# Optimization experiments

Hardware: AMD Instinct MI355X
Metric: run time of the kernel (lower is better)

Reference implementation:

```python
import jax, jax.numpy as jnp
import numpy as np

B, D, H = 4096, 128, 512


def _diffeq(t, y, W1, b1, v1, W2, b2):
    # y: [..., D] -> dy: [..., D]; time enters additively in the hidden layer
    h = jnp.tanh(y @ W1 + t * v1 + b1)
    return h @ W2 + b2


def setup_inputs() -> dict:
    key = jax.random.key(0)
    k = jax.random.split(key, 6)
    return {
        "t": jax.random.uniform(k[0], (), dtype=jnp.float32),
        "y": jax.random.normal(k[1], (B, D), dtype=jnp.float32),
        "logp": jnp.zeros((B, 1), dtype=jnp.float32),
        "W1": jax.random.normal(k[2], (D, H), dtype=jnp.float32) / np.sqrt(D),
        "b1": jnp.zeros((H,), dtype=jnp.float32),
        "v1": jax.random.normal(k[3], (H,), dtype=jnp.float32) / np.sqrt(H),
        "W2": jax.random.normal(k[4], (H, D), dtype=jnp.float32) / np.sqrt(H),
        "b2": jnp.zeros((D,), dtype=jnp.float32),
    }


def reference(t, y, logp, W1, b1, v1, W2, b2):
    # dy = diffeq(t, y)
    dy = _diffeq(t, y, W1, b1, v1, W2, b2)

    # Exact brute-force divergence: trace of per-sample Jacobian d(dy)/dy.
    # Original loops D autograd.grad passes; here a single vmapped jacfwd
    # (D forward-mode tangents) computes the same quantity.
    def f_single(yi):  # yi: [D]
        return _diffeq(t, yi, W1, b1, v1, W2, b2)

    jac = jax.vmap(jax.jacfwd(f_single))(y)          # [B, D, D]
    divergence = jnp.trace(jac, axis1=1, axis2=2)    # [B]
    divergence = divergence[:, None]                 # [B, 1]

    return (dy, -divergence)
```

## Files before the change

kernel.cpp:

```cpp
#include <hip/hip_runtime.h>

#define B_ 4096
#define D_ 128
#define H_ 512

typedef short v8s __attribute__((ext_vector_type(8)));
typedef float v4f __attribute__((ext_vector_type(4)));

__device__ __forceinline__ unsigned short f2bf(float f) {
    unsigned int u = __float_as_uint(f);
    u += 0x7fffu + ((u >> 16) & 1u);
    return (unsigned short)(u >> 16);
}

__global__ __launch_bounds__(256) void prep_kernel(
    const float* __restrict__ y, const float* __restrict__ W1,
    const float* __restrict__ W2,
    unsigned short* __restrict__ yb, unsigned short* __restrict__ W1T,
    unsigned short* __restrict__ W2T, float* __restrict__ s)
{
    __shared__ __align__(16) float smem[8448];
    const int tid = threadIdx.x;
    const int blk = blockIdx.x;

    if (blk < 64) {
        int idx = blk * 256 + tid;
#pragma unroll
        for (int i = 0; i < 8; ++i) {
            int e = idx + i * 16384;
            float4 v = ((const float4*)y)[e];
            ushort4 o;
            o.x = f2bf(v.x); o.y = f2bf(v.y); o.z = f2bf(v.z); o.w = f2bf(v.w);
            ((ushort4*)yb)[e] = o;
        }
    } else if (blk < 192) {
        float (*tile)[33] = (float(*)[33])smem;
        const float* src; unsigned short* dst;
        int srcC, dstC, r0, c0;
        if (blk < 128) {
            int tt = blk - 64;
            src = W1; dst = W1T; srcC = 512; dstC = 128;
            r0 = (tt >> 4) * 32; c0 = (tt & 15) * 32;
        } else {
            int tt = blk - 128;
            src = W2; dst = W2T; srcC = 128; dstC = 512;
            r0 = (tt >> 2) * 32; c0 = (tt & 3) * 32;
        }
        int c = tid & 31, r = tid >> 5;
#pragma unroll
        for (int i = 0; i < 4; ++i)
            tile[r + i * 8][c] = src[(r0 + r + i * 8) * srcC + c0 + c];
        __syncthreads();
        int rw = tid & 31, cw = tid >> 5;
#pragma unroll
        for (int i = 0; i < 4; ++i)
            dst[(c0 + cw + i * 8) * dstC + r0 + rw] = f2bf(tile[rw][cw + i * 8]);
    } else {
        int kbase = (blk - 192) * 64;
        for (int e = tid; e < 8192; e += 256) {
            int kk = e >> 7, i = e & 127;
            smem[kk * 132 + i] = W2[(kbase + kk) * 128 + i];
        }
        __syncthreads();
        int kk = tid >> 2, sub = tid & 3;
        int k = kbase + kk;
        float a = 0.f;
#pragma unroll 8
        for (int j = 0; j < 32; ++j) {
            int i = sub * 32 + j;
            a = fmaf(W1[i * H_ + k], smem[kk * 132 + i], a);
        }
        a += __shfl_xor(a, 1, 64);
        a += __shfl_xor(a, 2, 64);
        if (sub == 0) s[k] = a;
    }
}

__global__ __launch_bounds__(256) void ode_mfma(
    const float* __restrict__ t_, const unsigned short* __restrict__ yb,
    const unsigned short* __restrict__ W1T, const unsigned short* __restrict__ W2T,
    const float* __restrict__ sg, const float* __restrict__ b1g,
    const float* __restrict__ v1g, const float* __restrict__ b2g,
    float* __restrict__ out)
{
    __shared__ __align__(16) unsigned short hsm[16 * 520];
    __shared__ float divp[4][16];

    const int tid  = threadIdx.x;
    const int lane = tid & 63;
    const int wv   = tid >> 6;
    const int m    = lane & 15;
    const int quad = lane >> 4;
    const int row0 = blockIdx.x * 16;
    const float t  = t_[0];

    v8s af[4];
    const v8s* yrow = (const v8s*)&yb[(row0 + m) * D_ + quad * 8];
#pragma unroll
    for (int kki = 0; kki < 4; ++kki) af[kki] = yrow[kki * 4];

    float dacc[4] = {0.f, 0.f, 0.f, 0.f};

#pragma unroll 2
    for (int i = 0; i < 8; ++i) {
        const int n = (wv * 8 + i) * 16 + m;
        const v8s* wp = (const v8s*)&W1T[n * D_ + quad * 8];
        v8s bf0 = wp[0], bf1 = wp[4], bf2 = wp[8], bf3 = wp[12];
        v4f acc = {0.f, 0.f, 0.f, 0.f};
        acc = __builtin_amdgcn_mfma_f32_16x16x32_bf16(af[0], bf0, acc, 0, 0, 0);
        acc = __builtin_amdgcn_mfma_f32_16x16x32_bf16(af[1], bf1, acc, 0, 0, 0);
        acc = __builtin_amdgcn_mfma_f32_16x16x32_bf16(af[2], bf2, acc, 0, 0, 0);
        acc = __builtin_amdgcn_mfma_f32_16x16x32_bf16(af[3], bf3, acc, 0, 0, 0);

        const float pre = fmaf(t, v1g[n], b1g[n]);
        const float sk  = sg[n];
#pragma unroll
        for (int reg = 0; reg < 4; ++reg) {
            float x  = acc[reg] + pre;
            float e  = __expf(2.f * x);
            float th = 1.f - 2.f * __builtin_amdgcn_rcpf(e + 1.f);
            hsm[(quad * 4 + reg) * 520 + n] = f2bf(th);
            dacc[reg] = fmaf(1.f - th * th, sk, dacc[reg]);
        }
    }

#pragma unroll
    for (int reg = 0; reg < 4; ++reg) {
        float v = dacc[reg];
        v += __shfl_xor(v, 1, 64);
        v += __shfl_xor(v, 2, 64);
        v += __shfl_xor(v, 4, 64);
        v += __shfl_xor(v, 8, 64);
        dacc[reg] = v;
    }
    if (m == 0) {
#pragma unroll
        for (int reg = 0; reg < 4; ++reg) divp[wv][quad * 4 + reg] = dacc[reg];
    }
    __syncthreads();

    if (tid < 16) {
        float dv = divp[0][tid] + divp[1][tid] + divp[2][tid] + divp[3][tid];
        out[B_ * D_ + row0 + tid] = -dv;
    }

    const int d0 = wv * 32;
    const int dA = d0 + m, dB = d0 + 16 + m;
    v4f acc0 = {0.f, 0.f, 0.f, 0.f}, acc1 = {0.f, 0.f, 0.f, 0.f};
    const v8s* hrow = (const v8s*)&hsm[m * 520 + quad * 8];
    const v8s* w2a  = (const v8s*)&W2T[dA * H_ + quad * 8];
    const v8s* w2b  = (const v8s*)&W2T[dB * H_ + quad * 8];
#pragma unroll 4
    for (int kki = 0; kki < 16; ++kki) {
        v8s a  = hrow[kki * 4];
        v8s b0 = w2a[kki * 4];
        v8s b1 = w2b[kki * 4];
        acc0 = __builtin_amdgcn_mfma_f32_16x16x32_bf16(a, b0, acc0, 0, 0, 0);
        acc1 = __builtin_amdgcn_mfma_f32_16x16x32_bf16(a, b1, acc1, 0, 0, 0);
    }
    const float be0 = b2g[dA], be1 = b2g[dB];
#pragma unroll
    for (int reg = 0; reg < 4; ++reg) {
        const int r = row0 + quad * 4 + reg;
        out[r * D_ + dA] = acc0[reg] + be0;
        out[r * D_ + dB] = acc1[reg] + be1;
    }
}

extern "C" void kernel_launch(void* const* d_in, const int* in_sizes, int n_in,
                              void* d_out, int out_size, void* d_ws, size_t ws_size,
                              hipStream_t stream) {
    const float* t  = (const float*)d_in[0];
    const float* y  = (const float*)d_in[1];
    const float* W1 = (const float*)d_in[3];
    const float* b1 = (const float*)d_in[4];
    const float* v1 = (const float*)d_in[5];
    const float* W2 = (const float*)d_in[6];
    const float* b2 = (const float*)d_in[7];
    float* out = (float*)d_out;

    char* ws = (char*)d_ws;
    unsigned short* yb  = (unsigned short*)(ws);
    unsigned short* W1T = (unsigned short*)(ws + 1048576);
    unsigned short* W2T = (unsigned short*)(ws + 1179648);
    float*          s   = (float*)(ws + 1310720);

    prep_kernel<<<200, 256, 0, stream>>>(y, W1, W2, yb, W1T, W2T, s);
    ode_mfma<<<B_ / 16, 256, 0, stream>>>(t, yb, W1T, W2T, s, b1, v1, b2, out);
}
```

Before: 83.38 us.

## Fuse y bf16 conversion into main kernel and use 512-thread blocks

```diff
diff --git a/kernel.cpp b/kernel.cpp
--- a/kernel.cpp
+++ b/kernel.cpp
@@ -13,36 +13,34 @@
     return (unsigned short)(u >> 16);
 }
 
+__device__ __forceinline__ v8s cvt8(float4 a, float4 b) {
+    v8s r;
+    r[0] = (short)f2bf(a.x); r[1] = (short)f2bf(a.y);
+    r[2] = (short)f2bf(a.z); r[3] = (short)f2bf(a.w);
+    r[4] = (short)f2bf(b.x); r[5] = (short)f2bf(b.y);
+    r[6] = (short)f2bf(b.z); r[7] = (short)f2bf(b.w);
+    return r;
+}
+
 __global__ __launch_bounds__(256) void prep_kernel(
-    const float* __restrict__ y, const float* __restrict__ W1,
-    const float* __restrict__ W2,
-    unsigned short* __restrict__ yb, unsigned short* __restrict__ W1T,
-    unsigned short* __restrict__ W2T, float* __restrict__ s)
+    const float* __restrict__ W1, const float* __restrict__ W2,
+    unsigned short* __restrict__ W1T, unsigned short* __restrict__ W2T,
+    float* __restrict__ s)
 {
     __shared__ __align__(16) float smem[8448];
     const int tid = threadIdx.x;
     const int blk = blockIdx.x;
 
-    if (blk < 64) {
-        int idx = blk * 256 + tid;
-#pragma unroll
-        for (int i = 0; i < 8; ++i) {
-            int e = idx + i * 16384;
-            float4 v = ((const float4*)y)[e];
-            ushort4 o;
-            o.x = f2bf(v.x); o.y = f2bf(v.y); o.z = f2bf(v.z); o.w = f2bf(v.w);
-            ((ushort4*)yb)[e] = o;
-        }
-    } else if (blk < 192) {
+    if (blk < 128) {
         float (*tile)[33] = (float(*)[33])smem;
         const float* src; unsigned short* dst;
         int srcC, dstC, r0, c0;
-        if (blk < 128) {
-            int tt = blk - 64;
+        if (blk < 64) {
+            int tt = blk;
             src = W1; dst = W1T; srcC = 512; dstC = 128;
             r0 = (tt >> 4) * 32; c0 = (tt & 15) * 32;
         } else {
-            int tt = blk - 128;
+            int tt = blk - 64;
             src = W2; dst = W2T; srcC = 128; dstC = 512;
             r0 = (tt >> 2) * 32; c0 = (tt & 3) * 32;
         }
@@ -56,7 +54,7 @@
         for (int i = 0; i < 4; ++i)
             dst[(c0 + cw + i * 8) * dstC + r0 + rw] = f2bf(tile[rw][cw + i * 8]);
     } else {
-        int kbase = (blk - 192) * 64;
+        int kbase = (blk - 128) * 64;
         for (int e = tid; e < 8192; e += 256) {
             int kk = e >> 7, i = e & 127;
             smem[kk * 132 + i] = W2[(kbase + kk) * 128 + i];
@@ -76,15 +74,15 @@
     }
 }
 
-__global__ __launch_bounds__(256) void ode_mfma(
-    const float* __restrict__ t_, const unsigned short* __restrict__ yb,
+__global__ __launch_bounds__(512) void ode_mfma(
+    const float* __restrict__ t_, const float* __restrict__ y,
     const unsigned short* __restrict__ W1T, const unsigned short* __restrict__ W2T,
     const float* __restrict__ sg, const float* __restrict__ b1g,
     const float* __restrict__ v1g, const float* __restrict__ b2g,
     float* __restrict__ out)
 {
     __shared__ __align__(16) unsigned short hsm[16 * 520];
-    __shared__ float divp[4][16];
+    __shared__ float divp[8][16];
 
     const int tid  = threadIdx.x;
     const int lane = tid & 63;
@@ -95,25 +93,31 @@
     const float t  = t_[0];
 
     v8s af[4];
-    const v8s* yrow = (const v8s*)&yb[(row0 + m) * D_ + quad * 8];
-#pragma unroll
-    for (int kki = 0; kki < 4; ++kki) af[kki] = yrow[kki * 4];
+    {
+        const float4* yrow = (const float4*)&y[(row0 + m) * D_];
+#pragma unroll
+        for (int kki = 0; kki < 4; ++kki) {
+            float4 a = yrow[kki * 8 + quad * 2];
+            float4 b = yrow[kki * 8 + quad * 2 + 1];
+            af[kki] = cvt8(a, b);
+        }
+    }
 
     float dacc[4] = {0.f, 0.f, 0.f, 0.f};
 
 #pragma unroll 2
-    for (int i = 0; i < 8; ++i) {
-        const int n = (wv * 8 + i) * 16 + m;
+    for (int i = 0; i < 4; ++i) {
+        const int n = (wv * 4 + i) * 16 + m;
         const v8s* wp = (const v8s*)&W1T[n * D_ + quad * 8];
         v8s bf0 = wp[0], bf1 = wp[4], bf2 = wp[8], bf3 = wp[12];
+        const float pre = fmaf(t, v1g[n], b1g[n]);
+        const float sk  = sg[n];
         v4f acc = {0.f, 0.f, 0.f, 0.f};
         acc = __builtin_amdgcn_mfma_f32_16x16x32_bf16(af[0], bf0, acc, 0, 0, 0);
         acc = __builtin_amdgcn_mfma_f32_16x16x32_bf16(af[1], bf1, acc, 0, 0, 0);
         acc = __builtin_amdgcn_mfma_f32_16x16x32_bf16(af[2], bf2, acc, 0, 0, 0);
         acc = __builtin_amdgcn_mfma_f32_16x16x32_bf16(af[3], bf3, acc, 0, 0, 0);
 
-        const float pre = fmaf(t, v1g[n], b1g[n]);
-        const float sk  = sg[n];
 #pragma unroll
         for (int reg = 0; reg < 4; ++reg) {
             float x  = acc[reg] + pre;
@@ -137,33 +141,40 @@
 #pragma unroll
         for (int reg = 0; reg < 4; ++reg) divp[wv][quad * 4 + reg] = dacc[reg];
     }
+
+    const int d = wv * 16 + m;
+    const v8s* w2p_ = (const v8s*)&W2T[d * H_ + quad * 8];
+    const float be = b2g[d];
+    v8s w2p[8];
+#pragma unroll
+    for (int kki = 0; kki < 8; ++kki) w2p[kki] = w2p_[kki * 4];
+
     __syncthreads();
 
     if (tid < 16) {
-        float dv = divp[0][tid] + divp[1][tid] + divp[2][tid] + divp[3][tid];
+        float dv = 0.f;
+#pragma unroll
+        for (int w = 0; w < 8; ++w) dv += divp[w][tid];
         out[B_ * D_ + row0 + tid] = -dv;
     }
 
-    const int d0 = wv * 32;
-    const int dA = d0 + m, dB = d0 + 16 + m;
-    v4f acc0 = {0.f, 0.f, 0.f, 0.f}, acc1 = {0.f, 0.f, 0.f, 0.f};
+    v4f acc2 = {0.f, 0.f, 0.f, 0.f};
     const v8s* hrow = (const v8s*)&hsm[m * 520 + quad * 8];
-    const v8s* w2a  = (const v8s*)&W2T[dA * H_ + quad * 8];
-    const v8s* w2b  = (const v8s*)&W2T[dB * H_ + quad * 8];
-#pragma unroll 4
-    for (int kki = 0; kki < 16; ++kki) {
-        v8s a  = hrow[kki * 4];
-        v8s b0 = w2a[kki * 4];
-        v8s b1 = w2b[kki * 4];
-        acc0 = __builtin_amdgcn_mfma_f32_16x16x32_bf16(a, b0, acc0, 0, 0, 0);
-        acc1 = __builtin_amdgcn_mfma_f32_16x16x32_bf16(a, b1, acc1, 0, 0, 0);
-    }
-    const float be0 = b2g[dA], be1 = b2g[dB];
+#pragma unroll
+    for (int kki = 0; kki < 8; ++kki) {
+        v8s a = hrow[kki * 4];
+        acc2 = __builtin_amdgcn_mfma_f32_16x16x32_bf16(a, w2p[kki], acc2, 0, 0, 0);
+    }
+#pragma unroll
+    for (int kki = 8; kki < 16; ++kki) {
+        v8s a = hrow[kki * 4];
+        v8s b = w2p_[kki * 4];
+        acc2 = __builtin_amdgcn_mfma_f32_16x16x32_bf16(a, b, acc2, 0, 0, 0);
+    }
 #pragma unroll
     for (int reg = 0; reg < 4; ++reg) {
         const int r = row0 + quad * 4 + reg;
-        out[r * D_ + dA] = acc0[reg] + be0;
-        out[r * D_ + dB] = acc1[reg] + be1;
+        out[r * D_ + d] = acc2[reg] + be;
     }
 }
 
@@ -180,11 +191,10 @@
     float* out = (float*)d_out;
 
     char* ws = (char*)d_ws;
-    unsigned short* yb  = (unsigned short*)(ws);
-    unsigned short* W1T = (unsigned short*)(ws + 1048576);
-    unsigned short* W2T = (unsigned short*)(ws + 1179648);
-    float*          s   = (float*)(ws + 1310720);
-
-    prep_kernel<<<200, 256, 0, stream>>>(y, W1, W2, yb, W1T, W2T, s);
-    ode_mfma<<<B_ / 16, 256, 0, stream>>>(t, yb, W1T, W2T, s, b1, v1, b2, out);
-}
+    unsigned short* W1T = (unsigned short*)(ws);
+    unsigned short* W2T = (unsigned short*)(ws + 131072);
+    float*          s   = (float*)(ws + 262144);
+
+    prep_kernel<<<136, 256, 0, stream>>>(W1, W2, W1T, W2T, s);
+    ode_mfma<<<B_ / 16, 512, 0, stream>>>(t, y, W1T, W2T, s, b1, v1, b2, out);
+}
```

After: 83.33 us. About the same (-0.1%).
